# Kernel tuning notes

Hardware: AMD Instinct MI355X
Metric: run time of the kernel (lower is better)

The kernel has to match this reference:

```python
import jax, jax.numpy as jnp
import numpy as np

B, T, D, H = 8, 1024, 1024, 16
HD = D // H
SCALE = HD ** -0.5


def setup_inputs() -> dict:
    key = jax.random.key(0)
    ks = jax.random.split(key, 5)
    s = 0.02
    return {
        "hidden_states": jax.random.normal(ks[0], (B, T, D), jnp.float32),
        "Wq": jax.random.normal(ks[1], (D, D), jnp.float32) * s,
        "bq": jnp.zeros((D,), jnp.float32),
        "Wk": jax.random.normal(ks[2], (D, D), jnp.float32) * s,
        "bk": jnp.zeros((D,), jnp.float32),
        "Wv": jax.random.normal(ks[3], (D, D), jnp.float32) * s,
        "bv": jnp.zeros((D,), jnp.float32),
        "Wo": jax.random.normal(ks[4], (D, D), jnp.float32) * s,
        "bo": jnp.zeros((D,), jnp.float32),
    }


def _split_heads(x):
    # [B, T, D] -> [B, H, T, HD]
    return x.reshape(B, T, H, HD).transpose(0, 2, 1, 3)


def reference(hidden_states, Wq, bq, Wk, bk, Wv, bv, Wo, bo):
    q = _split_heads((hidden_states @ Wq + bq) * SCALE)
    k = _split_heads(hidden_states @ Wk + bk)
    v = _split_heads(hidden_states @ Wv + bv)
    # [B, H, T, T] attention scores
    scores = jnp.einsum("bhqd,bhkd->bhqk", q, k)
    probs = jax.nn.softmax(scores, axis=-1)
    attn = jnp.einsum("bhqk,bhkd->bhqd", probs, v)
    attn = attn.transpose(0, 2, 1, 3).reshape(B, T, D)
    return attn @ Wo + bo
```

## Files before the change

kernel.cpp:

```cpp
#include <hip/hip_runtime.h>

typedef unsigned short u16;
typedef __attribute__((ext_vector_type(4))) float f32x4;
typedef __attribute__((ext_vector_type(8))) __bf16 bf16x8;
typedef __attribute__((ext_vector_type(4))) __bf16 bf16x4;
typedef __attribute__((ext_vector_type(4))) unsigned short u16x4;
typedef __attribute__((ext_vector_type(8))) unsigned short u16x8;

static __device__ __forceinline__ u16 f2bf(float f) {
    union { float f; unsigned u; } v; v.f = f;
    unsigned r = v.u + 0x7FFFu + ((v.u >> 16) & 1u);
    return (u16)(r >> 16);
}

static __device__ __forceinline__ float exp2f_fast(float x) {
    float r; asm("v_exp_f32 %0, %1" : "=v"(r) : "v"(x)); return r;
}

static __device__ __forceinline__ void gload16(const u16* g, u16* l) {
    __builtin_amdgcn_global_load_lds(
        (const __attribute__((address_space(1))) unsigned int*)g,
        (__attribute__((address_space(3))) unsigned int*)l, 16, 0, 0);
}

#define WAIT_BAR() asm volatile("s_waitcnt vmcnt(0)\n\ts_barrier" ::: "memory")

template<int N> static __device__ __forceinline__ void vm_wait() {
    if constexpr (N >= 8)      asm volatile("s_waitcnt vmcnt(8)" ::: "memory");
    else if constexpr (N == 6) asm volatile("s_waitcnt vmcnt(6)" ::: "memory");
    else if constexpr (N == 4) asm volatile("s_waitcnt vmcnt(4)" ::: "memory");
    else if constexpr (N == 3) asm volatile("s_waitcnt vmcnt(3)" ::: "memory");
    else                       asm volatile("s_waitcnt vmcnt(0)" ::: "memory");
}

#define SWZ64(row, ec) (((row) * 64) + ((((ec) ^ ((row) & 7))) << 3))

__global__ __launch_bounds__(256) void k_cvt(const float* __restrict__ in, u16* __restrict__ out) {
    size_t i = (size_t)blockIdx.x * 256 + threadIdx.x;
    float4 v = ((const float4*)in)[i];
    u16x4 o; o[0] = f2bf(v.x); o[1] = f2bf(v.y); o[2] = f2bf(v.z); o[3] = f2bf(v.w);
    *(u16x4*)(out + i * 4) = o;
}

__global__ __launch_bounds__(256) void k_wtrans4(
    const float* __restrict__ W0, const float* __restrict__ W1,
    const float* __restrict__ W2, const float* __restrict__ W3,
    u16* __restrict__ T0, u16* __restrict__ T1, u16* __restrict__ T2, u16* __restrict__ T3,
    float s0) {
    const float* W; u16* Tt; float sc;
    switch (blockIdx.z) {
        case 0:  W = W0; Tt = T0; sc = s0;  break;
        case 1:  W = W1; Tt = T1; sc = 1.f; break;
        case 2:  W = W2; Tt = T2; sc = 1.f; break;
        default: W = W3; Tt = T3; sc = 1.f; break;
    }
    __shared__ float tile[32][33];
    int n0 = blockIdx.x * 32, k0 = blockIdx.y * 32;
    int tid = threadIdx.x;
    int r = tid >> 3, c = (tid & 7) * 4;
    float4 v = *(const float4*)(W + (size_t)(k0 + r) * 1024 + n0 + c);
    tile[r][c] = v.x; tile[r][c + 1] = v.y; tile[r][c + 2] = v.z; tile[r][c + 3] = v.w;
    __syncthreads();
    u16x4 o;
    o[0] = f2bf(tile[c][r] * sc);
    o[1] = f2bf(tile[c + 1][r] * sc);
    o[2] = f2bf(tile[c + 2][r] * sc);
    o[3] = f2bf(tile[c + 3][r] * sc);
    *(u16x4*)(Tt + (size_t)(n0 + r) * 1024 + k0 + c) = o;
}

template<int BN>
__global__ __launch_bounds__(512, 2) void k_g256(
    const u16* __restrict__ A, const u16* __restrict__ Bt,
    const float* __restrict__ bias, const float* __restrict__ biasK, float qscale,
    u16* __restrict__ obf, u16* __restrict__ obK, float* __restrict__ of32,
    int ldc, int bias_row, int nblk, int mode) {
    constexpr int WN = (BN == 256) ? 4 : 2;
    constexpr int WAVE_M = (BN == 256) ? 128 : 64;
    constexpr int M_REP = WAVE_M / 16;
    constexpr int BCALLS = BN / 128;
    constexpr int LPT = 2 + BCALLS;
    constexpr int ASLOT = 256 * 32;
    constexpr int BSLOT = BN * 32;
    __shared__ u16 As[4 * ASLOT];
    __shared__ u16 Bs[4 * BSLOT];
    const int tid = threadIdx.x;
    const int l = tid & 63, w = tid >> 6;
    const int mw = w / WN, nw = w % WN;
    const int fr = l & 15, gg = l >> 4, f4 = gg * 4;
    const int id = blockIdx.x;
    const int swz = (id & 7) * 32 + (id >> 3);
    const int bm = swz / nblk, bn = swz % nblk;
    const size_t m0 = (size_t)bm * 256, n0v = (size_t)bn * BN;

    const int srow = w * 16 + (l >> 2);
    const int schk = ((l & 3) ^ ((l >> 3) & 3)) * 8;
    const u16* agp0 = A + (m0 + srow) * 1024 + schk;
    const u16* agp1 = A + (m0 + 128 + srow) * 1024 + schk;
    const u16* bgp0 = Bt + (n0v + srow) * 1024 + schk;
    const u16* bgp1 = (BN == 256) ? Bt + (n0v + 128 + srow) * 1024 + schk : bgp0;
    const int ldst = w * 512 + l * 8;

    const int fchk = (gg ^ ((fr >> 1) & 3)) * 8;
    int aoff[8], boff[4];
#pragma unroll
    for (int mt = 0; mt < 8; ++mt) aoff[mt] = (mw * WAVE_M + mt * 16 + fr) * 32 + fchk;
#pragma unroll
    for (int nt = 0; nt < 4; ++nt) boff[nt] = (nw * 64 + nt * 16 + fr) * 32 + fchk;

    f32x4 acc[8][4] = {};

#define PSTG(S, J)                                                              \
    gload16(agp0 + (size_t)(J) * 32, As + (S) * ASLOT + ldst);                  \
    gload16(agp1 + (size_t)(J) * 32, As + (S) * ASLOT + 4096 + ldst);           \
    gload16(bgp0 + (size_t)(J) * 32, Bs + (S) * BSLOT + ldst);                  \
    if constexpr (BN == 256)                                                    \
        gload16(bgp1 + (size_t)(J) * 32, Bs + (S) * BSLOT + 4096 + ldst);
    PSTG(0, 0) PSTG(1, 1) PSTG(2, 2)
#undef PSTG

#define TILE(S, J, VMN, STG)                                                    \
    {                                                                           \
        vm_wait<VMN>();                                                         \
        __builtin_amdgcn_s_barrier();                                           \
        bf16x8 afr[4], bfr[4];                                                  \
        _Pragma("unroll")                                                       \
        for (int nt = 0; nt < 4; ++nt)                                          \
            bfr[nt] = *(const bf16x8*)(&Bs[(S) * BSLOT + boff[nt]]);            \
        _Pragma("unroll")                                                       \
        for (int mt = 0; mt < 4; ++mt)                                          \
            afr[mt] = *(const bf16x8*)(&As[(S) * ASLOT + aoff[mt]]);            \
        if constexpr (STG) {                                                    \
            gload16(agp0 + (size_t)((J) + 3) * 32, As + (((S) + 3) & 3) * ASLOT + ldst);        \
            gload16(agp1 + (size_t)((J) + 3) * 32, As + (((S) + 3) & 3) * ASLOT + 4096 + ldst); \
            if constexpr (BN == 128)                                            \
                gload16(bgp0 + (size_t)((J) + 3) * 32, Bs + (((S) + 3) & 3) * BSLOT + ldst);    \
        }                                                                       \
        __builtin_amdgcn_s_barrier();                                           \
        asm volatile("s_waitcnt lgkmcnt(0)" ::: "memory");                      \
        __builtin_amdgcn_sched_barrier(0);                                      \
        __builtin_amdgcn_s_setprio(1);                                          \
        _Pragma("unroll")                                                       \
        for (int mt = 0; mt < 4; ++mt)                                          \
            _Pragma("unroll")                                                   \
            for (int nt = 0; nt < 4; ++nt)                                      \
                acc[mt][nt] = __builtin_amdgcn_mfma_f32_16x16x32_bf16(afr[mt], bfr[nt], acc[mt][nt], 0, 0, 0); \
        __builtin_amdgcn_s_setprio(0);                                          \
        if constexpr (BN == 256) {                                              \
            _Pragma("unroll")                                                   \
            for (int mt = 0; mt < 4; ++mt)                                      \
                afr[mt] = *(const bf16x8*)(&As[(S) * ASLOT + aoff[4 + mt]]);    \
            if constexpr (STG) {                                                \
                gload16(bgp0 + (size_t)((J) + 3) * 32, Bs + (((S) + 3) & 3) * BSLOT + ldst);        \
                gload16(bgp1 + (size_t)((J) + 3) * 32, Bs + (((S) + 3) & 3) * BSLOT + 4096 + ldst); \
            }                                                                   \
            __builtin_amdgcn_s_barrier();                                       \
            asm volatile("s_waitcnt lgkmcnt(0)" ::: "memory");                  \
            __builtin_amdgcn_sched_barrier(0);                                  \
            __builtin_amdgcn_s_setprio(1);                                      \
            _Pragma("unroll")                                                   \
            for (int mt = 0; mt < 4; ++mt)                                      \
                _Pragma("unroll")                                               \
                for (int nt = 0; nt < 4; ++nt)                                  \
                    acc[4 + mt][nt] = __builtin_amdgcn_mfma_f32_16x16x32_bf16(afr[mt], bfr[nt], acc[4 + mt][nt], 0, 0, 0); \
            __builtin_amdgcn_s_setprio(0);                                      \
        }                                                                       \
    }

#pragma unroll 1
    for (int jb = 0; jb < 28; jb += 4) {
        TILE(0, jb + 0, (2 * LPT), true)
        TILE(1, jb + 1, (2 * LPT), true)
        TILE(2, jb + 2, (2 * LPT), true)
        TILE(3, jb + 3, (2 * LPT), true)
    }
    TILE(0, 28, (2 * LPT), true)
    TILE(1, 29, (2 * LPT), false)
    TILE(2, 30, LPT, false)
    TILE(3, 31, 0, false)
#undef TILE

    const int mrow0 = (int)m0 + mw * WAVE_M;
    const int ncol0 = (int)n0v + nw * 64;
    if (mode == 1) {
#pragma unroll
        for (int mt = 0; mt < M_REP; ++mt)
#pragma unroll
            for (int nt = 0; nt < 4; ++nt) {
                const int col = ncol0 + nt * 16 + fr;
                const int seg = col >> 10, colm = col & 1023;
                const float bb = (seg ? biasK[colm] : bias[colm] * qscale);
                u16* op = seg ? obK : obf;
#pragma unroll
                for (int r = 0; r < 4; ++r)
                    op[(size_t)(mrow0 + mt * 16 + f4 + r) * 1024 + colm] = f2bf(acc[mt][nt][r] + bb);
            }
    } else {
#pragma unroll
        for (int mt = 0; mt < M_REP; ++mt) {
            float rb_[4];
#pragma unroll
            for (int r = 0; r < 4; ++r)
                rb_[r] = bias_row ? bias[mrow0 + mt * 16 + f4 + r] : 0.f;
#pragma unroll
            for (int nt = 0; nt < 4; ++nt) {
                const int col = ncol0 + nt * 16 + fr;
                const float cb = bias_row ? 0.f : bias[col];
#pragma unroll
                for (int r = 0; r < 4; ++r) {
                    const size_t row = (size_t)(mrow0 + mt * 16 + f4 + r);
                    const float vv = acc[mt][nt][r] + cb + rb_[r];
                    if (of32) of32[row * (size_t)ldc + col] = vv;
                    else      obf[row * (size_t)ldc + col] = f2bf(vv);
                }
            }
        }
    }
}

static __device__ __forceinline__ void softmax_grp(const f32x4 s[4], f32x4 o[4],
                                                   float& m, float& lsum, bf16x4 p[4]) {
    float mymax = s[0][0];
#pragma unroll
    for (int nt = 0; nt < 4; ++nt)
#pragma unroll
        for (int r = 0; r < 4; ++r) mymax = fmaxf(mymax, s[nt][r]);
    float ps = 0.f;
#pragma unroll
    for (int nt = 0; nt < 4; ++nt)
#pragma unroll
        for (int r = 0; r < 4; ++r) {
            const float pp = exp2f_fast(s[nt][r]);
            ps += pp; p[nt][r] = (__bf16)pp;
        }
    if (__builtin_expect(__any(mymax > 11.0f), 0)) {
        float rm = fmaxf(mymax, __shfl_xor(mymax, 16, 64));
        rm = fmaxf(rm, __shfl_xor(rm, 32, 64));
        const float d = fmaxf(rm, 0.f);
        const float fac = exp2f_fast(-d);
        m += d; lsum *= fac;
#pragma unroll
        for (int mt = 0; mt < 4; ++mt)
#pragma unroll
            for (int r = 0; r < 4; ++r) o[mt][r] *= fac;
        ps = 0.f;
#pragma unroll
        for (int nt = 0; nt < 4; ++nt)
#pragma unroll
            for (int r = 0; r < 4; ++r) {
                const float pp = exp2f_fast(s[nt][r] - d);
                ps += pp; p[nt][r] = (__bf16)pp;
            }
    }
    lsum += ps;
}

static __device__ __forceinline__ void flash_tile(const u16* Ks, const u16* Vs,
                                                  int fr, int gg,
                                                  bf16x8 qA0, bf16x8 qA1, bf16x8 qB0, bf16x8 qB1,
                                                  f32x4 oA[4], f32x4 oB[4],
                                                  float& mA, float& lA, float& mB, float& lB) {
    f32x4 sA[4], sB[4];
    __builtin_amdgcn_s_setprio(1);
#pragma unroll
    for (int nt = 0; nt < 4; ++nt) {
        const int rk = nt * 16 + fr;
        const bf16x8 kf0 = *(const bf16x8*)(&Ks[SWZ64(rk, gg)]);
        const bf16x8 kf1 = *(const bf16x8*)(&Ks[SWZ64(rk, gg + 4)]);
        f32x4 z = {-mA, -mA, -mA, -mA};
        z = __builtin_amdgcn_mfma_f32_16x16x32_bf16(kf0, qA0, z, 0, 0, 0);
        z = __builtin_amdgcn_mfma_f32_16x16x32_bf16(kf1, qA1, z, 0, 0, 0);
        sA[nt] = z;
        f32x4 y = {-mB, -mB, -mB, -mB};
        y = __builtin_amdgcn_mfma_f32_16x16x32_bf16(kf0, qB0, y, 0, 0, 0);
        y = __builtin_amdgcn_mfma_f32_16x16x32_bf16(kf1, qB1, y, 0, 0, 0);
        sB[nt] = y;
    }
    __builtin_amdgcn_s_setprio(0);
    bf16x4 pA[4], pB[4];
    softmax_grp(sA, oA, mA, lA, pA);
    softmax_grp(sB, oB, mB, lB, pB);
    const bf16x8 BA0 = __builtin_shufflevector(pA[0], pA[1], 0, 1, 2, 3, 4, 5, 6, 7);
    const bf16x8 BA1 = __builtin_shufflevector(pA[2], pA[3], 0, 1, 2, 3, 4, 5, 6, 7);
    const bf16x8 BB0 = __builtin_shufflevector(pB[0], pB[1], 0, 1, 2, 3, 4, 5, 6, 7);
    const bf16x8 BB1 = __builtin_shufflevector(pB[2], pB[3], 0, 1, 2, 3, 4, 5, 6, 7);
    const int e0 = gg >> 1, hf = (gg & 1) * 4;
    __builtin_amdgcn_s_setprio(1);
#pragma unroll
    for (int mt = 0; mt < 4; ++mt) {
        const int rv = mt * 16 + fr;
        const int rs = rv & 7, rb = rv * 64;
        const bf16x4 v0 = *(const bf16x4*)(&Vs[rb + (((e0    ) ^ rs) << 3) + hf]);
        const bf16x4 v1 = *(const bf16x4*)(&Vs[rb + (((e0 + 2) ^ rs) << 3) + hf]);
        const bf16x4 v2 = *(const bf16x4*)(&Vs[rb + (((e0 + 4) ^ rs) << 3) + hf]);
        const bf16x4 v3 = *(const bf16x4*)(&Vs[rb + (((e0 + 6) ^ rs) << 3) + hf]);
        const bf16x8 vk0 = __builtin_shufflevector(v0, v1, 0, 1, 2, 3, 4, 5, 6, 7);
        const bf16x8 vk1 = __builtin_shufflevector(v2, v3, 0, 1, 2, 3, 4, 5, 6, 7);
        oA[mt] = __builtin_amdgcn_mfma_f32_16x16x32_bf16(vk0, BA0, oA[mt], 0, 0, 0);
        oA[mt] = __builtin_amdgcn_mfma_f32_16x16x32_bf16(vk1, BA1, oA[mt], 0, 0, 0);
        oB[mt] = __builtin_amdgcn_mfma_f32_16x16x32_bf16(vk0, BB0, oB[mt], 0, 0, 0);
        oB[mt] = __builtin_amdgcn_mfma_f32_16x16x32_bf16(vk1, BB1, oB[mt], 0, 0, 0);
    }
    __builtin_amdgcn_s_setprio(0);
}

__global__ __launch_bounds__(256, 2) void k_flash(const u16* __restrict__ Q, const u16* __restrict__ K,
                                                  const u16* __restrict__ Vt2, u16* __restrict__ O) {
    __shared__ u16 Ks0[64 * 64], Vs0[64 * 64];
    __shared__ u16 Ks1[64 * 64], Vs1[64 * 64];
    const int tid = threadIdx.x;
    const int l = tid & 63, w = tid >> 6;
    const int id = blockIdx.x;
    const int swz = (id & 7) * 128 + (id >> 3);
    const int bh = swz >> 3, qt = swz & 7;
    const int b = bh >> 4, h = bh & 15;
    const int qw = qt * 128 + w * 32;
    const int fr = l & 15, gg = l >> 4, f4 = gg * 4, f8 = gg * 8;

    const u16* qpA = Q + ((size_t)(b * 1024 + qw + fr)) * 1024 + h * 64 + f8;
    const u16* qpB = qpA + 16 * 1024;
    const bf16x8 qA0 = *(const bf16x8*)qpA;
    const bf16x8 qA1 = *(const bf16x8*)(qpA + 32);
    const bf16x8 qB0 = *(const bf16x8*)qpB;
    const bf16x8 qB1 = *(const bf16x8*)(qpB + 32);

    const int jj0 = w * 2, jj1 = w * 2 + 1;
    const int sr0 = jj0 * 8 + (l >> 3), sr1 = jj1 * 8 + (l >> 3);
    const int sc = ((l & 7) ^ (l >> 3)) * 8;
    const u16* kg0 = K + ((size_t)(b * 1024 + sr0)) * 1024 + h * 64 + sc;
    const u16* kg1 = K + ((size_t)(b * 1024 + sr1)) * 1024 + h * 64 + sc;
    const u16* vg0 = Vt2 + ((size_t)(h * 64 + sr0)) * 8192 + b * 1024 + sc;
    const u16* vg1 = Vt2 + ((size_t)(h * 64 + sr1)) * 8192 + b * 1024 + sc;
    const int lk0 = jj0 * 512 + l * 8, lk1 = jj1 * 512 + l * 8;

#define FSTAGE(KSB, VSB, kt)                            \
    gload16(kg0 + (size_t)(kt) * 1024, (KSB) + lk0);    \
    gload16(kg1 + (size_t)(kt) * 1024, (KSB) + lk1);    \
    gload16(vg0 + (kt), (VSB) + lk0);                   \
    gload16(vg1 + (kt), (VSB) + lk1)

    f32x4 oA[4] = {}, oB[4] = {};
    float mA = 0.f, lA = 0.f, mB = 0.f, lB = 0.f;

    FSTAGE(Ks0, Vs0, 0);
    WAIT_BAR();
    for (int kt0 = 0; kt0 < 1024; kt0 += 128) {
        if (kt0 + 64 < 1024) { FSTAGE(Ks1, Vs1, kt0 + 64); }
        flash_tile(Ks0, Vs0, fr, gg, qA0, qA1, qB0, qB1, oA, oB, mA, lA, mB, lB);
        WAIT_BAR();
        if (kt0 + 128 < 1024) { FSTAGE(Ks0, Vs0, kt0 + 128); }
        flash_tile(Ks1, Vs1, fr, gg, qA0, qA1, qB0, qB1, oA, oB, mA, lA, mB, lB);
        WAIT_BAR();
    }
#undef FSTAGE
    lA += __shfl_xor(lA, 16, 64); lA += __shfl_xor(lA, 32, 64);
    lB += __shfl_xor(lB, 16, 64); lB += __shfl_xor(lB, 32, 64);
    const float ivA = 1.0f / lA, ivB = 1.0f / lB;
    u16* opA = O + ((size_t)(b * 1024 + qw + fr)) * 1024 + h * 64;
    u16* opB = opA + 16 * 1024;
#pragma unroll
    for (int mt = 0; mt < 4; ++mt) {
        u16x4 oa, ob;
#pragma unroll
        for (int r = 0; r < 4; ++r) { oa[r] = f2bf(oA[mt][r] * ivA); ob[r] = f2bf(oB[mt][r] * ivB); }
        *(u16x4*)(opA + mt * 16 + f4) = oa;
        *(u16x4*)(opB + mt * 16 + f4) = ob;
    }
}

extern "C" void kernel_launch(void* const* d_in, const int* in_sizes, int n_in,
                              void* d_out, int out_size, void* d_ws, size_t ws_size,
                              hipStream_t stream) {
    (void)in_sizes; (void)n_in; (void)out_size; (void)ws_size;
    const float* hs = (const float*)d_in[0];
    const float* Wq = (const float*)d_in[1];
    const float* bq = (const float*)d_in[2];
    const float* Wk = (const float*)d_in[3];
    const float* bk = (const float*)d_in[4];
    const float* Wv = (const float*)d_in[5];
    const float* bv = (const float*)d_in[6];
    const float* Wo = (const float*)d_in[7];
    const float* bo = (const float*)d_in[8];
    float* out = (float*)d_out;
    char* ws = (char*)d_ws;
    const size_t MB = 1024ull * 1024ull;
    u16* Xb  = (u16*)(ws);
    u16* Wqt = (u16*)(ws + 16 * MB);
    u16* Wkt = (u16*)(ws + 18 * MB);
    u16* Wvt = (u16*)(ws + 20 * MB);
    u16* Wot = (u16*)(ws + 22 * MB);
    u16* Qb  = (u16*)(ws + 24 * MB);
    u16* Kb  = (u16*)(ws + 40 * MB);
    u16* Vt2 = (u16*)(ws + 56 * MB);
    u16* Ob  = Xb;

    const float SCALE_Q = 0.125f * 1.4426950408889634f;

    k_cvt<<<dim3(8192), dim3(256), 0, stream>>>(hs, Xb);
    k_wtrans4<<<dim3(32, 32, 4), dim3(256), 0, stream>>>(Wq, Wk, Wv, Wo, Wqt, Wkt, Wvt, Wot, SCALE_Q);
    k_g256<256><<<dim3(256), dim3(512), 0, stream>>>(Xb, Wqt, bq, bk, SCALE_Q,
                                                     Qb, Kb, nullptr, 1024, 0, 8, 1);
    k_g256<128><<<dim3(256), dim3(512), 0, stream>>>(Wvt, Xb, bv, nullptr, 1.f,
                                                     Vt2, nullptr, nullptr, 8192, 1, 64, 0);
    k_flash<<<dim3(1024), dim3(256), 0, stream>>>(Qb, Kb, Vt2, Ob);
    k_g256<128><<<dim3(256), dim3(512), 0, stream>>>(Ob, Wot, bo, nullptr, 1.f,
                                                     nullptr, nullptr, out, 1024, 0, 8, 0);
}
```

Measured before the change: 155.8 us.

## Software-pipeline flash loop with 4-stage buffers and permuted V layout

Restructures the flash attention loop into a fully unrolled 4-buffer pipeline that overlaps the QK^T of tile T with the PV of tile T-1. Loads are issued two tiles ahead with partial vmcnt waits instead of draining to zero each iteration. The V projection epilogue also writes V in a permuted column order, so the flash kernel reads V fragments as single 16-byte LDS loads instead of four 8-byte loads plus shuffles. The cost is doubled LDS use (64KB per block), which may limit occupancy at 2 blocks per CU, and more registers for the carried P tiles.

```diff
diff --git a/kernel.cpp b/kernel.cpp
--- a/kernel.cpp
+++ b/kernel.cpp
@@ -22,8 +22,6 @@
         (const __attribute__((address_space(1))) unsigned int*)g,
         (__attribute__((address_space(3))) unsigned int*)l, 16, 0, 0);
 }
-
-#define WAIT_BAR() asm volatile("s_waitcnt vmcnt(0)\n\ts_barrier" ::: "memory")
 
 template<int N> static __device__ __forceinline__ void vm_wait() {
     if constexpr (N >= 8)      asm volatile("s_waitcnt vmcnt(8)" ::: "memory");
@@ -195,6 +193,24 @@
                 for (int r = 0; r < 4; ++r)
                     op[(size_t)(mrow0 + mt * 16 + f4 + r) * 1024 + colm] = f2bf(acc[mt][nt][r] + bb);
             }
+    } else if (mode == 2) {
+#pragma unroll
+        for (int mt = 0; mt < M_REP; ++mt) {
+            float rb_[4];
+#pragma unroll
+            for (int r = 0; r < 4; ++r) rb_[r] = bias[mrow0 + mt * 16 + f4 + r];
+#pragma unroll
+            for (int nt = 0; nt < 4; ++nt) {
+                const int col = ncol0 + nt * 16 + fr;
+                const int colp = (col & ~31) | (((col >> 2) & 3) << 3) |
+                                 (((col >> 4) & 1) << 2) | (col & 3);
+#pragma unroll
+                for (int r = 0; r < 4; ++r) {
+                    const size_t row = (size_t)(mrow0 + mt * 16 + f4 + r);
+                    obf[row * (size_t)ldc + colp] = f2bf(acc[mt][nt][r] + rb_[r]);
+                }
+            }
+        }
     } else {
 #pragma unroll
         for (int mt = 0; mt < M_REP; ++mt) {
@@ -218,49 +234,9 @@
     }
 }
 
-static __device__ __forceinline__ void softmax_grp(const f32x4 s[4], f32x4 o[4],
-                                                   float& m, float& lsum, bf16x4 p[4]) {
-    float mymax = s[0][0];
-#pragma unroll
-    for (int nt = 0; nt < 4; ++nt)
-#pragma unroll
-        for (int r = 0; r < 4; ++r) mymax = fmaxf(mymax, s[nt][r]);
-    float ps = 0.f;
-#pragma unroll
-    for (int nt = 0; nt < 4; ++nt)
-#pragma unroll
-        for (int r = 0; r < 4; ++r) {
-            const float pp = exp2f_fast(s[nt][r]);
-            ps += pp; p[nt][r] = (__bf16)pp;
-        }
-    if (__builtin_expect(__any(mymax > 11.0f), 0)) {
-        float rm = fmaxf(mymax, __shfl_xor(mymax, 16, 64));
-        rm = fmaxf(rm, __shfl_xor(rm, 32, 64));
-        const float d = fmaxf(rm, 0.f);
-        const float fac = exp2f_fast(-d);
-        m += d; lsum *= fac;
-#pragma unroll
-        for (int mt = 0; mt < 4; ++mt)
-#pragma unroll
-            for (int r = 0; r < 4; ++r) o[mt][r] *= fac;
-        ps = 0.f;
-#pragma unroll
-        for (int nt = 0; nt < 4; ++nt)
-#pragma unroll
-            for (int r = 0; r < 4; ++r) {
-                const float pp = exp2f_fast(s[nt][r] - d);
-                ps += pp; p[nt][r] = (__bf16)pp;
-            }
-    }
-    lsum += ps;
-}
-
-static __device__ __forceinline__ void flash_tile(const u16* Ks, const u16* Vs,
-                                                  int fr, int gg,
-                                                  bf16x8 qA0, bf16x8 qA1, bf16x8 qB0, bf16x8 qB1,
-                                                  f32x4 oA[4], f32x4 oB[4],
-                                                  float& mA, float& lA, float& mB, float& lB) {
-    f32x4 sA[4], sB[4];
+static __device__ __forceinline__ void qk_tile(const u16* Ks, int fr, int gg,
+                                               bf16x8 qA0, bf16x8 qA1, bf16x8 qB0, bf16x8 qB1,
+                                               float mA, float mB, f32x4 sA[4], f32x4 sB[4]) {
     __builtin_amdgcn_s_setprio(1);
 #pragma unroll
     for (int nt = 0; nt < 4; ++nt) {
@@ -277,25 +253,58 @@
         sB[nt] = y;
     }
     __builtin_amdgcn_s_setprio(0);
-    bf16x4 pA[4], pB[4];
-    softmax_grp(sA, oA, mA, lA, pA);
-    softmax_grp(sB, oB, mB, lB, pB);
+}
+
+static __device__ __forceinline__ void sm_tile(const f32x4 s[4], f32x4 o[4],
+                                               float& m, float& lsum, bf16x4 p[4]) {
+    float mymax = s[0][0];
+#pragma unroll
+    for (int nt = 0; nt < 4; ++nt)
+#pragma unroll
+        for (int r = 0; r < 4; ++r) mymax = fmaxf(mymax, s[nt][r]);
+    float ps = 0.f;
+#pragma unroll
+    for (int nt = 0; nt < 4; ++nt)
+#pragma unroll
+        for (int r = 0; r < 4; ++r) {
+            const float pp = exp2f_fast(s[nt][r]);
+            ps += pp; p[nt][r] = (__bf16)pp;
+        }
+    if (__builtin_expect(__any(mymax > 11.0f), 0)) {
+        float rm = fmaxf(mymax, __shfl_xor(mymax, 16, 64));
+        rm = fmaxf(rm, __shfl_xor(rm, 32, 64));
+        const float d = fmaxf(rm, 0.f);
+        const float fac = exp2f_fast(-d);
+        m += d; lsum *= fac;
+#pragma unroll
+        for (int mt = 0; mt < 4; ++mt)
+#pragma unroll
+            for (int r = 0; r < 4; ++r) o[mt][r] *= fac;
+        ps = 0.f;
+#pragma unroll
+        for (int nt = 0; nt < 4; ++nt)
+#pragma unroll
+            for (int r = 0; r < 4; ++r) {
+                const float pp = exp2f_fast(s[nt][r] - d);
+                ps += pp; p[nt][r] = (__bf16)pp;
+            }
+    }
+    lsum += ps;
+}
+
+static __device__ __forceinline__ void pv_tile(const u16* Vs, int fr, int gg,
+                                               const bf16x4 pA[4], const bf16x4 pB[4],
+                                               f32x4 oA[4], f32x4 oB[4]) {
     const bf16x8 BA0 = __builtin_shufflevector(pA[0], pA[1], 0, 1, 2, 3, 4, 5, 6, 7);
     const bf16x8 BA1 = __builtin_shufflevector(pA[2], pA[3], 0, 1, 2, 3, 4, 5, 6, 7);
     const bf16x8 BB0 = __builtin_shufflevector(pB[0], pB[1], 0, 1, 2, 3, 4, 5, 6, 7);
     const bf16x8 BB1 = __builtin_shufflevector(pB[2], pB[3], 0, 1, 2, 3, 4, 5, 6, 7);
-    const int e0 = gg >> 1, hf = (gg & 1) * 4;
     __builtin_amdgcn_s_setprio(1);
 #pragma unroll
     for (int mt = 0; mt < 4; ++mt) {
         const int rv = mt * 16 + fr;
-        const int rs = rv & 7, rb = rv * 64;
-        const bf16x4 v0 = *(const bf16x4*)(&Vs[rb + (((e0    ) ^ rs) << 3) + hf]);
-        const bf16x4 v1 = *(const bf16x4*)(&Vs[rb + (((e0 + 2) ^ rs) << 3) + hf]);
-        const bf16x4 v2 = *(const bf16x4*)(&Vs[rb + (((e0 + 4) ^ rs) << 3) + hf]);
-        const bf16x4 v3 = *(const bf16x4*)(&Vs[rb + (((e0 + 6) ^ rs) << 3) + hf]);
-        const bf16x8 vk0 = __builtin_shufflevector(v0, v1, 0, 1, 2, 3, 4, 5, 6, 7);
-        const bf16x8 vk1 = __builtin_shufflevector(v2, v3, 0, 1, 2, 3, 4, 5, 6, 7);
+        const bf16x8 vk0 = *(const bf16x8*)(&Vs[SWZ64(rv, gg)]);
+        const bf16x8 vk1 = *(const bf16x8*)(&Vs[SWZ64(rv, gg + 4)]);
         oA[mt] = __builtin_amdgcn_mfma_f32_16x16x32_bf16(vk0, BA0, oA[mt], 0, 0, 0);
         oA[mt] = __builtin_amdgcn_mfma_f32_16x16x32_bf16(vk1, BA1, oA[mt], 0, 0, 0);
         oB[mt] = __builtin_amdgcn_mfma_f32_16x16x32_bf16(vk0, BB0, oB[mt], 0, 0, 0);
@@ -306,8 +315,8 @@
 
 __global__ __launch_bounds__(256, 2) void k_flash(const u16* __restrict__ Q, const u16* __restrict__ K,
                                                   const u16* __restrict__ Vt2, u16* __restrict__ O) {
-    __shared__ u16 Ks0[64 * 64], Vs0[64 * 64];
-    __shared__ u16 Ks1[64 * 64], Vs1[64 * 64];
+    __shared__ u16 Ks[4][64 * 64];
+    __shared__ u16 Vs[4][64 * 64];
     const int tid = threadIdx.x;
     const int l = tid & 63, w = tid >> 6;
     const int id = blockIdx.x;
@@ -333,26 +342,50 @@
     const u16* vg1 = Vt2 + ((size_t)(h * 64 + sr1)) * 8192 + b * 1024 + sc;
     const int lk0 = jj0 * 512 + l * 8, lk1 = jj1 * 512 + l * 8;
 
-#define FSTAGE(KSB, VSB, kt)                            \
-    gload16(kg0 + (size_t)(kt) * 1024, (KSB) + lk0);    \
-    gload16(kg1 + (size_t)(kt) * 1024, (KSB) + lk1);    \
-    gload16(vg0 + (kt), (VSB) + lk0);                   \
-    gload16(vg1 + (kt), (VSB) + lk1)
+#define FSTG(S, kt)                                         \
+    gload16(kg0 + (size_t)(kt) * 1024, Ks[S] + lk0);        \
+    gload16(kg1 + (size_t)(kt) * 1024, Ks[S] + lk1);        \
+    gload16(vg0 + (kt), Vs[S] + lk0);                       \
+    gload16(vg1 + (kt), Vs[S] + lk1);
 
     f32x4 oA[4] = {}, oB[4] = {};
     float mA = 0.f, lA = 0.f, mB = 0.f, lB = 0.f;
-
-    FSTAGE(Ks0, Vs0, 0);
-    WAIT_BAR();
-    for (int kt0 = 0; kt0 < 1024; kt0 += 128) {
-        if (kt0 + 64 < 1024) { FSTAGE(Ks1, Vs1, kt0 + 64); }
-        flash_tile(Ks0, Vs0, fr, gg, qA0, qA1, qB0, qB1, oA, oB, mA, lA, mB, lB);
-        WAIT_BAR();
-        if (kt0 + 128 < 1024) { FSTAGE(Ks0, Vs0, kt0 + 128); }
-        flash_tile(Ks1, Vs1, fr, gg, qA0, qA1, qB0, qB1, oA, oB, mA, lA, mB, lB);
-        WAIT_BAR();
-    }
-#undef FSTAGE
+    bf16x4 p0A[4], p0B[4], p1A[4], p1B[4];
+
+    FSTG(0, 0) FSTG(1, 64)
+
+#define FITER(T, PCA, PCB, PPA, PPB, VMN, DOPV)                              \
+    {                                                                        \
+        vm_wait<VMN>();                                                      \
+        __builtin_amdgcn_s_barrier();                                        \
+        f32x4 sA[4], sB[4];                                                  \
+        qk_tile(Ks[(T) & 3], fr, gg, qA0, qA1, qB0, qB1, mA, mB, sA, sB);    \
+        if ((T) + 2 <= 15) { FSTG((((T) + 2) & 3), ((T) + 2) * 64) }         \
+        if (DOPV) pv_tile(Vs[((T) - 1) & 3], fr, gg, PPA, PPB, oA, oB);      \
+        sm_tile(sA, oA, mA, lA, PCA);                                        \
+        sm_tile(sB, oB, mB, lB, PCB);                                        \
+    }
+
+    FITER(0,  p0A, p0B, p1A, p1B, 4, false)
+    FITER(1,  p1A, p1B, p0A, p0B, 4, true)
+    FITER(2,  p0A, p0B, p1A, p1B, 4, true)
+    FITER(3,  p1A, p1B, p0A, p0B, 4, true)
+    FITER(4,  p0A, p0B, p1A, p1B, 4, true)
+    FITER(5,  p1A, p1B, p0A, p0B, 4, true)
+    FITER(6,  p0A, p0B, p1A, p1B, 4, true)
+    FITER(7,  p1A, p1B, p0A, p0B, 4, true)
+    FITER(8,  p0A, p0B, p1A, p1B, 4, true)
+    FITER(9,  p1A, p1B, p0A, p0B, 4, true)
+    FITER(10, p0A, p0B, p1A, p1B, 4, true)
+    FITER(11, p1A, p1B, p0A, p0B, 4, true)
+    FITER(12, p0A, p0B, p1A, p1B, 4, true)
+    FITER(13, p1A, p1B, p0A, p0B, 4, true)
+    FITER(14, p0A, p0B, p1A, p1B, 4, true)
+    FITER(15, p1A, p1B, p0A, p0B, 0, true)
+#undef FITER
+#undef FSTG
+    pv_tile(Vs[3], fr, gg, p1A, p1B, oA, oB);
+
     lA += __shfl_xor(lA, 16, 64); lA += __shfl_xor(lA, 32, 64);
     lB += __shfl_xor(lB, 16, 64); lB += __shfl_xor(lB, 32, 64);
     const float ivA = 1.0f / lA, ivB = 1.0f / lB;
@@ -401,7 +434,7 @@
     k_g256<256><<<dim3(256), dim3(512), 0, stream>>>(Xb, Wqt, bq, bk, SCALE_Q,
                                                      Qb, Kb, nullptr, 1024, 0, 8, 1);
     k_g256<128><<<dim3(256), dim3(512), 0, stream>>>(Wvt, Xb, bv, nullptr, 1.f,
-                                                     Vt2, nullptr, nullptr, 8192, 1, 64, 0);
+                                                     Vt2, nullptr, nullptr, 8192, 1, 64, 2);
     k_flash<<<dim3(1024), dim3(256), 0, stream>>>(Qb, Kb, Vt2, Ob);
     k_g256<128><<<dim3(256), dim3(512), 0, stream>>>(Ob, Wot, bo, nullptr, 1.f,
                                                      nullptr, nullptr, out, 1024, 0, 8, 0);
```

Result: faster. 150.8 us (-3.2%).
